# Kernel tuning notes

Measured on AMD Instinct MI355X. Metric: run time of the kernel, lower is better.

## Reference

```python
import jax, jax.numpy as jnp
import numpy as np

N_CONS = 100000
N_VARS = 200000
N_EDGES = 2000000
EMB = 64


def _emb(x, w0, b0, w1, b1):
    # Linear -> ReLU -> Linear -> ReLU
    h = jnp.maximum(x @ w0 + b0, 0.0)
    return jnp.maximum(h @ w1 + b1, 0.0)


def _bgc(left, src, dst, ef, right, lw, lb, ew, rw, fw, fb, ow0, ob0, ow1, ob1):
    # message: final(ReLU)(left_lin(right[dst]) + edge_lin(ef) + right_lin(left[src]))
    pre = right[dst] @ lw + lb + ef @ ew + left[src] @ rw          # [E, EMB]
    msg = jnp.maximum(pre, 0.0) @ fw + fb                          # [E, EMB]
    agg = jax.ops.segment_sum(msg, dst, num_segments=right.shape[0])  # [n_right, EMB]
    h = jnp.concatenate([agg, right], axis=-1)                     # [n_right, 2*EMB]
    return jnp.maximum(h @ ow0 + ob0, 0.0) @ ow1 + ob1


def setup_inputs() -> dict:
    key = jax.random.key(0)
    kit = iter(jax.random.split(key, 64))
    f32 = jnp.float32
    def W(i, o):
        return (jax.random.normal(next(kit), (i, o), f32) / np.float32(np.sqrt(i))).astype(f32)
    def B(o):
        return jnp.zeros((o,), f32)

    d = {}
    d['constraint_features'] = jax.random.normal(next(kit), (N_CONS, 5), f32)
    ei_c = jax.random.randint(next(kit), (N_EDGES,), 0, N_CONS)
    ei_v = jax.random.randint(next(kit), (N_EDGES,), 0, N_VARS)
    d['edge_indices'] = jnp.stack([ei_c, ei_v]).astype(jnp.int32)  # [2, E]
    d['edge_features'] = jax.random.normal(next(kit), (N_EDGES, 1), f32)
    d['variable_features'] = jax.random.normal(next(kit), (N_VARS, 19), f32)

    # cons / var embeddings
    d['cw0'], d['cb0'], d['cw1'], d['cb1'] = W(5, EMB), B(EMB), W(EMB, EMB), B(EMB)
    d['vw0'], d['vb0'], d['vw1'], d['vb1'] = W(19, EMB), B(EMB), W(EMB, EMB), B(EMB)
    # two bipartite convs
    for p in ('vc', 'cv'):
        d[p + '_lw'], d[p + '_lb'] = W(EMB, EMB), B(EMB)
        d[p + '_ew'] = W(1, EMB)
        d[p + '_rw'] = W(EMB, EMB)
        d[p + '_fw'], d[p + '_fb'] = W(EMB, EMB), B(EMB)
        d[p + '_ow0'], d[p + '_ob0'] = W(2 * EMB, EMB), B(EMB)
        d[p + '_ow1'], d[p + '_ob1'] = W(EMB, EMB), B(EMB)
    # policy head (final Linear has no bias)
    d['pw0'], d['pb0'], d['pw1'] = W(EMB, EMB), B(EMB), W(EMB, 1)
    # value head
    d['vhw0'], d['vhb0'], d['vhw1'], d['vhb1'] = W(EMB, EMB), B(EMB), W(EMB, 1), B(1)
    return d


def reference(constraint_features, edge_indices, edge_features, variable_features,
              cw0, cb0, cw1, cb1, vw0, vb0, vw1, vb1,
              vc_lw, vc_lb, vc_ew, vc_rw, vc_fw, vc_fb, vc_ow0, vc_ob0, vc_ow1, vc_ob1,
              cv_lw, cv_lb, cv_ew, cv_rw, cv_fw, cv_fb, cv_ow0, cv_ob0, cv_ow1, cv_ob1,
              pw0, pb0, pw1, vhw0, vhb0, vhw1, vhb1):
    cons_idx = edge_indices[0]
    var_idx = edge_indices[1]
    c = _emb(constraint_features, cw0, cb0, cw1, cb1)  # [n_cons, EMB]
    v = _emb(variable_features, vw0, vb0, vw1, vb1)    # [n_vars, EMB]
    # v -> c (reversed edges: src=var, dst=cons)
    c = _bgc(v, var_idx, cons_idx, edge_features, c,
             vc_lw, vc_lb, vc_ew, vc_rw, vc_fw, vc_fb, vc_ow0, vc_ob0, vc_ow1, vc_ob1)
    # c -> v (src=cons, dst=var)
    v = _bgc(c, cons_idx, var_idx, edge_features, v,
             cv_lw, cv_lb, cv_ew, cv_rw, cv_fw, cv_fb, cv_ow0, cv_ob0, cv_ow1, cv_ob1)
    policy = (jnp.maximum(v @ pw0 + pb0, 0.0) @ pw1).squeeze(-1)   # [n_vars]
    value = (jnp.maximum(v @ vhw0 + vhb0, 0.0) @ vhw1 + vhb1).squeeze(-1)  # [n_vars]
    return (value, policy)
```

## Files before the change

### kernel.cpp

```cpp
#include <hip/hip_runtime.h>

typedef unsigned short u16;

__device__ __forceinline__ float bf2f(u16 u) {
    return __uint_as_float(((unsigned int)u) << 16);
}
__device__ __forceinline__ u16 f2bf(float f) {
    unsigned int x = __float_as_uint(f);
    return (u16)((x + 0x7fffu + ((x >> 16) & 1u)) >> 16);
}

__device__ __forceinline__ void mm64(const float* A, const float* B, float* C, int lane)
{
    float bcol[64];
#pragma unroll
    for (int m = 0; m < 64; ++m) bcol[m] = B[m*64 + lane];
    for (int k = 0; k < 64; ++k) {
        float acc = 0.f;
#pragma unroll
        for (int m = 0; m < 64; ++m) acc = fmaf(A[k*64 + m], bcol[m], acc);
        C[k*64 + lane] = acc;
    }
}

__device__ __forceinline__ void vm64(const float* a, const float* B, const float* add,
                                     float* c, int lane)
{
    float acc = (add != 0) ? add[lane] : 0.f;
#pragma unroll
    for (int m = 0; m < 64; ++m) acc = fmaf(a[m], B[m*64 + lane], acc);
    c[lane] = acc;
}

__global__ __launch_bounds__(256) void prep_kernel(
    const float* vc_fw, const float* vc_fb, const float* vc_ow0,
    const float* vc_ow1, const float* vc_ob1,
    const float* cv_rw, const float* cv_fw, const float* cv_fb,
    const float* cv_ow0, const float* cv_ow1, const float* cv_ob1,
    const float* pw0, const float* pb0, const float* vhw0, const float* vhb0,
    float* Fc, float* gc, float* Hc, float* hc, float* Fv, float* gv,
    float* Pw, float* pbp, float* Vw, float* vbp)
{
    const int wv = threadIdx.x >> 6;
    const int lane = threadIdx.x & 63;
    if (wv == 0) {
        mm64(vc_fw, vc_ow0, Fc, lane);
        vm64(vc_fb, vc_ow0, 0, gc, lane);
    } else if (wv == 1) {
        mm64(vc_ow1, cv_rw, Hc, lane);
        vm64(vc_ob1, cv_rw, 0, hc, lane);
    } else if (wv == 2) {
        mm64(cv_fw, cv_ow0, Fv, lane);
        vm64(cv_fb, cv_ow0, 0, gv, lane);
    } else {
        mm64(cv_ow1, pw0, Pw, lane);
        vm64(cv_ob1, pw0, pb0, pbp, lane);
        mm64(cv_ow1, vhw0, Vw, lane);
        vm64(cv_ob1, vhw0, vhb0, vbp, lane);
    }
}

__global__ __launch_bounds__(256) void embc_kernel(
    const float* __restrict__ X,
    const float* __restrict__ W0, const float* __restrict__ B0,
    const float* __restrict__ W1, const float* __restrict__ B1,
    const float* __restrict__ LW, const float* __restrict__ LB,
    u16* __restrict__ c0out, float* __restrict__ RlOut, int M)
{
    const int lane = threadIdx.x & 63;
    const int wv   = threadIdx.x >> 6;
    __shared__ __align__(16) float xs[4][8*5];
    __shared__ __align__(16) float hb[4][8][64];
    __shared__ __align__(16) float yb[4][8][64];
    const int rowTile = (blockIdx.x*4 + wv)*8;

    for (int idx = lane; idx < 8*5; idx += 64) {
        long gi = (long)rowTile*5 + idx;
        xs[wv][idx] = (gi < (long)M*5) ? X[gi] : 0.f;
    }
    {
        float w0[5];
#pragma unroll
        for (int k = 0; k < 5; ++k) w0[k] = W0[k*64 + lane];
        const float b0 = B0[lane];
#pragma unroll
        for (int r = 0; r < 8; ++r) {
            float acc = b0;
#pragma unroll
            for (int k = 0; k < 5; ++k) acc = fmaf(xs[wv][r*5 + k], w0[k], acc);
            hb[wv][r][lane] = fmaxf(acc, 0.f);
        }
    }
    {
        float w1[64];
#pragma unroll
        for (int k = 0; k < 64; ++k) w1[k] = W1[k*64 + lane];
        const float b1 = B1[lane];
#pragma unroll
        for (int r = 0; r < 8; ++r) {
            float acc = b1;
#pragma unroll
            for (int k4 = 0; k4 < 16; ++k4) {
                float4 h4 = *(const float4*)&hb[wv][r][k4*4];
                acc = fmaf(h4.x, w1[k4*4+0], acc);
                acc = fmaf(h4.y, w1[k4*4+1], acc);
                acc = fmaf(h4.z, w1[k4*4+2], acc);
                acc = fmaf(h4.w, w1[k4*4+3], acc);
            }
            float y = fmaxf(acc, 0.f);
            yb[wv][r][lane] = y;
            int row = rowTile + r;
            if (row < M) c0out[(size_t)row*64 + lane] = f2bf(y);
        }
    }
    {
        float w[64];
#pragma unroll
        for (int k = 0; k < 64; ++k) w[k] = LW[k*64 + lane];
        const float bb = LB[lane];
#pragma unroll
        for (int r = 0; r < 8; ++r) {
            float acc = bb;
#pragma unroll
            for (int k4 = 0; k4 < 16; ++k4) {
                float4 y4 = *(const float4*)&yb[wv][r][k4*4];
                acc = fmaf(y4.x, w[k4*4+0], acc);
                acc = fmaf(y4.y, w[k4*4+1], acc);
                acc = fmaf(y4.z, w[k4*4+2], acc);
                acc = fmaf(y4.w, w[k4*4+3], acc);
            }
            int row = rowTile + r;
            if (row < M) RlOut[(size_t)row*64 + lane] = acc;
        }
    }
}

__global__ __launch_bounds__(256) void embv_kernel(
    const float* __restrict__ X,
    const float* __restrict__ W0, const float* __restrict__ B0,
    const float* __restrict__ W1, const float* __restrict__ B1,
    const float* __restrict__ RW,
    const float* __restrict__ LW, const float* __restrict__ LB,
    u16* __restrict__ v0out, u16* __restrict__ LsOut,
    float* __restrict__ RlOut, int M)
{
    const int lane = threadIdx.x & 63;
    const int wv   = threadIdx.x >> 6;
    __shared__ __align__(16) float xs[4][8*19];
    __shared__ __align__(16) float hb[4][8][64];
    __shared__ __align__(16) float yb[4][8][64];
    const int rowTile = (blockIdx.x*4 + wv)*8;

    for (int idx = lane; idx < 8*19; idx += 64) {
        long gi = (long)rowTile*19 + idx;
        xs[wv][idx] = (gi < (long)M*19) ? X[gi] : 0.f;
    }
    {
        float w0[19];
#pragma unroll
        for (int k = 0; k < 19; ++k) w0[k] = W0[k*64 + lane];
        const float b0 = B0[lane];
#pragma unroll
        for (int r = 0; r < 8; ++r) {
            float acc = b0;
#pragma unroll
            for (int k = 0; k < 19; ++k) acc = fmaf(xs[wv][r*19 + k], w0[k], acc);
            hb[wv][r][lane] = fmaxf(acc, 0.f);
        }
    }
    {
        float w1[64];
#pragma unroll
        for (int k = 0; k < 64; ++k) w1[k] = W1[k*64 + lane];
        const float b1 = B1[lane];
#pragma unroll
        for (int r = 0; r < 8; ++r) {
            float acc = b1;
#pragma unroll
            for (int k4 = 0; k4 < 16; ++k4) {
                float4 h4 = *(const float4*)&hb[wv][r][k4*4];
                acc = fmaf(h4.x, w1[k4*4+0], acc);
                acc = fmaf(h4.y, w1[k4*4+1], acc);
                acc = fmaf(h4.z, w1[k4*4+2], acc);
                acc = fmaf(h4.w, w1[k4*4+3], acc);
            }
            float y = fmaxf(acc, 0.f);
            yb[wv][r][lane] = y;
            int row = rowTile + r;
            if (row < M) v0out[(size_t)row*64 + lane] = f2bf(y);
        }
    }
    {
        float w[64];
#pragma unroll
        for (int k = 0; k < 64; ++k) w[k] = RW[k*64 + lane];
#pragma unroll
        for (int r = 0; r < 8; ++r) {
            float acc = 0.f;
#pragma unroll
            for (int k4 = 0; k4 < 16; ++k4) {
                float4 y4 = *(const float4*)&yb[wv][r][k4*4];
                acc = fmaf(y4.x, w[k4*4+0], acc);
                acc = fmaf(y4.y, w[k4*4+1], acc);
                acc = fmaf(y4.z, w[k4*4+2], acc);
                acc = fmaf(y4.w, w[k4*4+3], acc);
            }
            int row = rowTile + r;
            if (row < M) LsOut[(size_t)row*64 + lane] = f2bf(acc);
        }
    }
    {
        float w[64];
#pragma unroll
        for (int k = 0; k < 64; ++k) w[k] = LW[k*64 + lane];
        const float bb = LB[lane];
#pragma unroll
        for (int r = 0; r < 8; ++r) {
            float acc = bb;
#pragma unroll
            for (int k4 = 0; k4 < 16; ++k4) {
                float4 y4 = *(const float4*)&yb[wv][r][k4*4];
                acc = fmaf(y4.x, w[k4*4+0], acc);
                acc = fmaf(y4.y, w[k4*4+1], acc);
                acc = fmaf(y4.z, w[k4*4+2], acc);
                acc = fmaf(y4.w, w[k4*4+3], acc);
            }
            int row = rowTile + r;
            if (row < M) RlOut[(size_t)row*64 + lane] = acc;
        }
    }
}

__global__ __launch_bounds__(256) void hist2_kernel(
    const int* __restrict__ eic, const int* __restrict__ eiv,
    int* cntC, int* cntV, int E)
{
    int e = blockIdx.x*256 + threadIdx.x;
    if (e >= E) return;
    atomicAdd(&cntC[eic[e]], 1);
    atomicAdd(&cntV[eiv[e]], 1);
}

__global__ __launch_bounds__(256) void scan1_kernel(const int* __restrict__ in, int* blks, int N)
{
    __shared__ int sm[256];
    const int t = threadIdx.x;
    const int base = blockIdx.x*1024 + t*4;
    int s = 0;
#pragma unroll
    for (int i = 0; i < 4; ++i) { int idx = base + i; if (idx < N) s += in[idx]; }
    sm[t] = s; __syncthreads();
    for (int d = 128; d > 0; d >>= 1) { if (t < d) sm[t] += sm[t + d]; __syncthreads(); }
    if (t == 0) blks[blockIdx.x] = sm[0];
}

__global__ __launch_bounds__(256) void scan2_kernel(const int* __restrict__ blks, int* blkex, int nb)
{
    __shared__ int sm[1024];
    for (int i = threadIdx.x; i < nb; i += 256) sm[i] = blks[i];
    __syncthreads();
    if (threadIdx.x == 0) { int a = 0; for (int i = 0; i < nb; ++i) { int v = sm[i]; sm[i] = a; a += v; } }
    __syncthreads();
    for (int i = threadIdx.x; i < nb; i += 256) blkex[i] = sm[i];
}

__global__ __launch_bounds__(256) void scan3_kernel(
    const int* __restrict__ in, const int* __restrict__ blkex, int* out, int N)
{
    __shared__ int sm[256];
    const int t = threadIdx.x;
    const int base = blockIdx.x*1024 + t*4;
    int v[4]; int s = 0;
#pragma unroll
    for (int i = 0; i < 4; ++i) { int idx = base + i; v[i] = (idx < N) ? in[idx] : 0; s += v[i]; }
    sm[t] = s; __syncthreads();
    int x = s;
    for (int d = 1; d < 256; d <<= 1) {
        int y = (t >= d) ? sm[t - d] : 0;
        __syncthreads();
        x += y; sm[t] = x;
        __syncthreads();
    }
    int off0 = blkex[blockIdx.x] + (x - s);
#pragma unroll
    for (int i = 0; i < 4; ++i) {
        int idx = base + i;
        if (idx < N) {
            out[idx] = off0;
            off0 += v[i];
            if (idx == N - 1) out[N] = off0;
        }
    }
}

__global__ __launch_bounds__(256) void scatter2_kernel(
    const int* __restrict__ eic, const int* __restrict__ eiv,
    const float* __restrict__ ef,
    int* curC, int* curV, float2* __restrict__ bC, float2* __restrict__ bV, int E)
{
    int e = blockIdx.x*256 + threadIdx.x;
    if (e >= E) return;
    const int c = eic[e], v = eiv[e];
    const float f = ef[e];
    int pc = atomicAdd(&curC[c], 1);
    bC[pc] = make_float2(__int_as_float(v), f);
    int pv = atomicAdd(&curV[v], 1);
    bV[pv] = make_float2(__int_as_float(c), f);
}

__global__ __launch_bounds__(256) void agg_kernel(
    const int* __restrict__ off, const float2* __restrict__ bucket,
    float* RlA, const u16* __restrict__ Lsb,
    const float* __restrict__ ew, int N)
{
    const int node = blockIdx.x*4 + (threadIdx.x >> 6);
    if (node >= N) return;
    const int lane = threadIdx.x & 63;
    const int s0 = off[node];
    const int e1 = off[node + 1];
    const float rl = RlA[(size_t)node*64 + lane];
    const float w  = ew[lane];

    float acc = 0.f;
    int j = s0;
    for (; j + 8 <= e1; j += 8) {
        float2 q0 = bucket[j+0], q1 = bucket[j+1], q2 = bucket[j+2], q3 = bucket[j+3];
        float2 q4 = bucket[j+4], q5 = bucket[j+5], q6 = bucket[j+6], q7 = bucket[j+7];
        float l0 = bf2f(Lsb[(size_t)__float_as_int(q0.x)*64 + lane]);
        float l1 = bf2f(Lsb[(size_t)__float_as_int(q1.x)*64 + lane]);
        float l2 = bf2f(Lsb[(size_t)__float_as_int(q2.x)*64 + lane]);
        float l3 = bf2f(Lsb[(size_t)__float_as_int(q3.x)*64 + lane]);
        float l4 = bf2f(Lsb[(size_t)__float_as_int(q4.x)*64 + lane]);
        float l5 = bf2f(Lsb[(size_t)__float_as_int(q5.x)*64 + lane]);
        float l6 = bf2f(Lsb[(size_t)__float_as_int(q6.x)*64 + lane]);
        float l7 = bf2f(Lsb[(size_t)__float_as_int(q7.x)*64 + lane]);
        acc += fmaxf(fmaf(q0.y, w, rl + l0), 0.f);
        acc += fmaxf(fmaf(q1.y, w, rl + l1), 0.f);
        acc += fmaxf(fmaf(q2.y, w, rl + l2), 0.f);
        acc += fmaxf(fmaf(q3.y, w, rl + l3), 0.f);
        acc += fmaxf(fmaf(q4.y, w, rl + l4), 0.f);
        acc += fmaxf(fmaf(q5.y, w, rl + l5), 0.f);
        acc += fmaxf(fmaf(q6.y, w, rl + l6), 0.f);
        acc += fmaxf(fmaf(q7.y, w, rl + l7), 0.f);
    }
    for (; j < e1; ++j) {
        float2 q = bucket[j];
        float l = bf2f(Lsb[(size_t)__float_as_int(q.x)*64 + lane]);
        acc += fmaxf(fmaf(q.y, w, rl + l), 0.f);
    }
    RlA[(size_t)node*64 + lane] = acc;
}

__global__ __launch_bounds__(256, 1) void consupd_kernel(
    const float* __restrict__ aggpre, const u16* __restrict__ c0,
    const int* __restrict__ off,
    const float* __restrict__ Fc, const float* __restrict__ OW0B,
    const float* __restrict__ gc, const float* __restrict__ ob0,
    const float* __restrict__ Hc, const float* __restrict__ hc,
    u16* __restrict__ LsOut, int M)
{
    const int lane = threadIdx.x & 63;
    const int wv   = threadIdx.x >> 6;
    __shared__ __align__(16) float xs[4][8][64];
    __shared__ __align__(16) float cs[4][8][64];
    const int rowTile = (blockIdx.x*4 + wv)*8;

    float degv[8];
#pragma unroll
    for (int r = 0; r < 8; ++r) {
        int row = rowTile + r;
        int grow = (row < M) ? row : (M - 1);
        xs[wv][r][lane] = aggpre[(size_t)grow*64 + lane];
        cs[wv][r][lane] = bf2f(c0[(size_t)grow*64 + lane]);
        degv[r] = (float)(off[grow + 1] - off[grow]);
    }
    {
        float wa[64], wb[64];
#pragma unroll
        for (int k = 0; k < 64; ++k) { wa[k] = Fc[k*64 + lane]; wb[k] = OW0B[k*64 + lane]; }
        const float g_l = gc[lane], b_l = ob0[lane];
#pragma unroll
        for (int r = 0; r < 8; ++r) {
            float acc = fmaf(degv[r], g_l, b_l);
#pragma unroll
            for (int k4 = 0; k4 < 16; ++k4) {
                float4 x4 = *(const float4*)&xs[wv][r][k4*4];
                float4 c4 = *(const float4*)&cs[wv][r][k4*4];
                acc = fmaf(x4.x, wa[k4*4+0], acc); acc = fmaf(c4.x, wb[k4*4+0], acc);
                acc = fmaf(x4.y, wa[k4*4+1], acc); acc = fmaf(c4.y, wb[k4*4+1], acc);
                acc = fmaf(x4.z, wa[k4*4+2], acc); acc = fmaf(c4.z, wb[k4*4+2], acc);
                acc = fmaf(x4.w, wa[k4*4+3], acc); acc = fmaf(c4.w, wb[k4*4+3], acc);
            }
            xs[wv][r][lane] = fmaxf(acc, 0.f);
        }
    }
    {
        float wh[64];
#pragma unroll
        for (int k = 0; k < 64; ++k) wh[k] = Hc[k*64 + lane];
        const float h_l = hc[lane];
#pragma unroll
        for (int r = 0; r < 8; ++r) {
            float acc = h_l;
#pragma unroll
            for (int k4 = 0; k4 < 16; ++k4) {
                float4 u4 = *(const float4*)&xs[wv][r][k4*4];
                acc = fmaf(u4.x, wh[k4*4+0], acc);
                acc = fmaf(u4.y, wh[k4*4+1], acc);
                acc = fmaf(u4.z, wh[k4*4+2], acc);
                acc = fmaf(u4.w, wh[k4*4+3], acc);
            }
            int row = rowTile + r;
            if (row < M) LsOut[(size_t)row*64 + lane] = f2bf(acc);
        }
    }
}

__global__ __launch_bounds__(256, 1) void varupdhead_kernel(
    const float* __restrict__ aggpre, const u16* __restrict__ v0,
    const int* __restrict__ off,
    const float* __restrict__ Fv, const float* __restrict__ OW0B,
    const float* __restrict__ gv, const float* __restrict__ ob0,
    const float* __restrict__ Pw, const float* __restrict__ pbp, const float* __restrict__ pw1,
    const float* __restrict__ Vw, const float* __restrict__ vbp, const float* __restrict__ vw1,
    const float* __restrict__ vb1,
    float* __restrict__ out, int M)
{
    const int lane = threadIdx.x & 63;
    const int wv   = threadIdx.x >> 6;
    __shared__ __align__(16) float xs[4][8][64];
    __shared__ __align__(16) float cs[4][8][64];
    const int rowTile = (blockIdx.x*4 + wv)*8;

    float degv[8];
#pragma unroll
    for (int r = 0; r < 8; ++r) {
        int row = rowTile + r;
        int grow = (row < M) ? row : (M - 1);
        xs[wv][r][lane] = aggpre[(size_t)grow*64 + lane];
        cs[wv][r][lane] = bf2f(v0[(size_t)grow*64 + lane]);
        degv[r] = (float)(off[grow + 1] - off[grow]);
    }
    {
        float wa[64], wb[64];
#pragma unroll
        for (int k = 0; k < 64; ++k) { wa[k] = Fv[k*64 + lane]; wb[k] = OW0B[k*64 + lane]; }
        const float g_l = gv[lane], b_l = ob0[lane];
#pragma unroll
        for (int r = 0; r < 8; ++r) {
            float acc = fmaf(degv[r], g_l, b_l);
#pragma unroll
            for (int k4 = 0; k4 < 16; ++k4) {
                float4 x4 = *(const float4*)&xs[wv][r][k4*4];
                float4 c4 = *(const float4*)&cs[wv][r][k4*4];
                acc = fmaf(x4.x, wa[k4*4+0], acc); acc = fmaf(c4.x, wb[k4*4+0], acc);
                acc = fmaf(x4.y, wa[k4*4+1], acc); acc = fmaf(c4.y, wb[k4*4+1], acc);
                acc = fmaf(x4.z, wa[k4*4+2], acc); acc = fmaf(c4.z, wb[k4*4+2], acc);
                acc = fmaf(x4.w, wa[k4*4+3], acc); acc = fmaf(c4.w, wb[k4*4+3], acc);
            }
            xs[wv][r][lane] = fmaxf(acc, 0.f);
        }
    }
    {
        float wp[64], wq[64];
#pragma unroll
        for (int k = 0; k < 64; ++k) { wp[k] = Pw[k*64 + lane]; wq[k] = Vw[k*64 + lane]; }
        const float pb_l = pbp[lane], vb_l = vbp[lane];
        const float p1w = pw1[lane], v1w = vw1[lane];
        const float vbias = vb1[0];
#pragma unroll
        for (int r = 0; r < 8; ++r) {
            float tp = pb_l, tv = vb_l;
#pragma unroll
            for (int k4 = 0; k4 < 16; ++k4) {
                float4 u4 = *(const float4*)&xs[wv][r][k4*4];
                tp = fmaf(u4.x, wp[k4*4+0], tp); tv = fmaf(u4.x, wq[k4*4+0], tv);
                tp = fmaf(u4.y, wp[k4*4+1], tp); tv = fmaf(u4.y, wq[k4*4+1], tv);
                tp = fmaf(u4.z, wp[k4*4+2], tp); tv = fmaf(u4.z, wq[k4*4+2], tv);
                tp = fmaf(u4.w, wp[k4*4+3], tp); tv = fmaf(u4.w, wq[k4*4+3], tv);
            }
            tp = fmaxf(tp, 0.f) * p1w;
            tv = fmaxf(tv, 0.f) * v1w;
#pragma unroll
            for (int m = 32; m >= 1; m >>= 1) {
                tp += __shfl_xor(tp, m, 64);
                tv += __shfl_xor(tv, m, 64);
            }
            int row = rowTile + r;
            if (lane == 0 && row < M) {
                out[row]     = tv + vbias;
                out[M + row] = tp;
            }
        }
    }
}

#define AL256(x) (((x) + 255) & ~(size_t)255)

extern "C" void kernel_launch(void* const* d_in, const int* in_sizes, int n_in,
                              void* d_out, int out_size, void* d_ws, size_t ws_size,
                              hipStream_t stream)
{
    const float* cf  = (const float*)d_in[0];
    const int*   ei  = (const int*)  d_in[1];
    const float* ef  = (const float*)d_in[2];
    const float* vf  = (const float*)d_in[3];

    const float* cw0 = (const float*)d_in[4];
    const float* cb0 = (const float*)d_in[5];
    const float* cw1 = (const float*)d_in[6];
    const float* cb1 = (const float*)d_in[7];
    const float* vw0 = (const float*)d_in[8];
    const float* vb0 = (const float*)d_in[9];
    const float* vw1 = (const float*)d_in[10];
    const float* vb1 = (const float*)d_in[11];

    const float* vc_lw  = (const float*)d_in[12];
    const float* vc_lb  = (const float*)d_in[13];
    const float* vc_ew  = (const float*)d_in[14];
    const float* vc_rw  = (const float*)d_in[15];
    const float* vc_fw  = (const float*)d_in[16];
    const float* vc_fb  = (const float*)d_in[17];
    const float* vc_ow0 = (const float*)d_in[18];
    const float* vc_ob0 = (const float*)d_in[19];
    const float* vc_ow1 = (const float*)d_in[20];
    const float* vc_ob1 = (const float*)d_in[21];

    const float* cv_lw  = (const float*)d_in[22];
    const float* cv_lb  = (const float*)d_in[23];
    const float* cv_ew  = (const float*)d_in[24];
    const float* cv_rw  = (const float*)d_in[25];
    const float* cv_fw  = (const float*)d_in[26];
    const float* cv_fb  = (const float*)d_in[27];
    const float* cv_ow0 = (const float*)d_in[28];
    const float* cv_ob0 = (const float*)d_in[29];
    const float* cv_ow1 = (const float*)d_in[30];
    const float* cv_ob1 = (const float*)d_in[31];

    const float* pw0  = (const float*)d_in[32];
    const float* pb0  = (const float*)d_in[33];
    const float* pw1  = (const float*)d_in[34];
    const float* vhw0 = (const float*)d_in[35];
    const float* vhb0 = (const float*)d_in[36];
    const float* vhw1 = (const float*)d_in[37];
    const float* vhb1 = (const float*)d_in[38];

    const int NC = in_sizes[0] / 5;
    const int E  = in_sizes[1] / 2;
    const int NV = in_sizes[3] / 19;
    const int* eic = ei;
    const int* eiv = ei + E;

    char* base = (char*)d_ws;
    size_t o = 0;
    float*  RlC = (float*)(base + o);  o += AL256((size_t)NC*64*4);
    u16*    c0b = (u16*)  (base + o);  o += AL256((size_t)NC*64*2);
    u16*    LsC = (u16*)  (base + o);  o += AL256((size_t)NC*64*2);
    float*  RlV = (float*)(base + o);  o += AL256((size_t)NV*64*4);
    u16*    v0b = (u16*)  (base + o);  o += AL256((size_t)NV*64*2);
    u16*    LsV = (u16*)  (base + o);  o += AL256((size_t)NV*64*2);
    float2* bktC = (float2*)(base + o); o += AL256((size_t)E*8);
    float2* bktV = (float2*)(base + o); o += AL256((size_t)E*8);
    int* cntC = (int*)(base + o);  o += AL256((size_t)NC*4);
    int* offC = (int*)(base + o);  o += AL256(((size_t)NC + 1)*4);
    int* cntV = (int*)(base + o);  o += AL256((size_t)NV*4);
    int* offV = (int*)(base + o);  o += AL256(((size_t)NV + 1)*4);
    int* blks = (int*)(base + o);  o += AL256((size_t)1024*4);
    int* blkex= (int*)(base + o);  o += AL256((size_t)1024*4);
    float* Fc  = (float*)(base + o); o += AL256((size_t)4096*4);
    float* Hc  = (float*)(base + o); o += AL256((size_t)4096*4);
    float* Fv  = (float*)(base + o); o += AL256((size_t)4096*4);
    float* Pw  = (float*)(base + o); o += AL256((size_t)4096*4);
    float* Vw  = (float*)(base + o); o += AL256((size_t)4096*4);
    float* gc  = (float*)(base + o); o += AL256((size_t)64*4);
    float* hc  = (float*)(base + o); o += AL256((size_t)64*4);
    float* gv  = (float*)(base + o); o += AL256((size_t)64*4);
    float* pbp = (float*)(base + o); o += AL256((size_t)64*4);
    float* vbp = (float*)(base + o); o += AL256((size_t)64*4);

    if (o > ws_size) return;

    dim3 blk(256);
    dim3 gRowsC((unsigned)((NC + 31) / 32));
    dim3 gRowsV((unsigned)((NV + 31) / 32));
    dim3 gNodeC((unsigned)((NC + 3) / 4));
    dim3 gNodeV((unsigned)((NV + 3) / 4));
    dim3 gE((unsigned)((E + 255) / 256));
    const int nbC = (NC + 1023) / 1024;
    const int nbV = (NV + 1023) / 1024;

    (void)hipMemsetAsync(cntC, 0, (size_t)NC*4, stream);
    (void)hipMemsetAsync(cntV, 0, (size_t)NV*4, stream);
    hist2_kernel<<<gE, blk, 0, stream>>>(eic, eiv, cntC, cntV, E);
    scan1_kernel<<<dim3(nbC), blk, 0, stream>>>(cntC, blks, NC);
    scan2_kernel<<<dim3(1),   blk, 0, stream>>>(blks, blkex, nbC);
    scan3_kernel<<<dim3(nbC), blk, 0, stream>>>(cntC, blkex, offC, NC);
    scan1_kernel<<<dim3(nbV), blk, 0, stream>>>(cntV, blks, NV);
    scan2_kernel<<<dim3(1),   blk, 0, stream>>>(blks, blkex, nbV);
    scan3_kernel<<<dim3(nbV), blk, 0, stream>>>(cntV, blkex, offV, NV);

    prep_kernel<<<dim3(1), blk, 0, stream>>>(
        vc_fw, vc_fb, vc_ow0, vc_ow1, vc_ob1,
        cv_rw, cv_fw, cv_fb, cv_ow0, cv_ow1, cv_ob1,
        pw0, pb0, vhw0, vhb0,
        Fc, gc, Hc, hc, Fv, gv, Pw, pbp, Vw, vbp);

    embc_kernel<<<gRowsC, blk, 0, stream>>>(cf, cw0, cb0, cw1, cb1,
                                            vc_lw, vc_lb, c0b, RlC, NC);
    embv_kernel<<<gRowsV, blk, 0, stream>>>(vf, vw0, vb0, vw1, vb1,
                                            vc_rw, cv_lw, cv_lb, v0b, LsV, RlV, NV);

    (void)hipMemcpyAsync(cntC, offC, (size_t)NC*4, hipMemcpyDeviceToDevice, stream);
    (void)hipMemcpyAsync(cntV, offV, (size_t)NV*4, hipMemcpyDeviceToDevice, stream);
    scatter2_kernel<<<gE, blk, 0, stream>>>(eic, eiv, ef, cntC, cntV, bktC, bktV, E);

    agg_kernel<<<gNodeC, blk, 0, stream>>>(offC, bktC, RlC, LsV, vc_ew, NC);
    consupd_kernel<<<gRowsC, blk, 0, stream>>>(RlC, c0b, offC,
                                               Fc, vc_ow0 + 64*64, gc, vc_ob0,
                                               Hc, hc, LsC, NC);

    agg_kernel<<<gNodeV, blk, 0, stream>>>(offV, bktV, RlV, LsC, cv_ew, NV);
    varupdhead_kernel<<<gRowsV, blk, 0, stream>>>(RlV, v0b, offV,
                                                  Fv, cv_ow0 + 64*64, gv, cv_ob0,
                                                  Pw, pbp, pw1, Vw, vbp, vhw1, vhb1,
                                                  (float*)d_out, NV);
}
```

Before: 1.216 ms.

## Replace per-node CSR with coarse 128-node buckets and LDS-atomic aggregation

Edges are now bucketed by groups of 128 destination nodes instead of being fully sorted per node. The multi-kernel prefix scan becomes one single-block coarse scan, and the scatter atomics go to far fewer counters. Aggregation runs one block per bucket and accumulates into shared memory with LDS atomics. The local node index is packed into the low 7 bits of the edge feature and rl is stored as bf16, which slightly lowers precision. LDS atomic contention and a single-block serial scan over roughly 1600 buckets are the added costs.

```diff
diff --git a/kernel.cpp b/kernel.cpp
--- a/kernel.cpp
+++ b/kernel.cpp
@@ -1,6 +1,9 @@
 #include <hip/hip_runtime.h>
 
 typedef unsigned short u16;
+
+#define RN  128
+#define RSH 7
 
 __device__ __forceinline__ float bf2f(u16 u) {
     return __uint_as_float(((unsigned int)u) << 16);
@@ -241,119 +244,117 @@
     atomicAdd(&cntV[eiv[e]], 1);
 }
 
-__global__ __launch_bounds__(256) void scan1_kernel(const int* __restrict__ in, int* blks, int N)
-{
-    __shared__ int sm[256];
-    const int t = threadIdx.x;
-    const int base = blockIdx.x*1024 + t*4;
-    int s = 0;
-#pragma unroll
-    for (int i = 0; i < 4; ++i) { int idx = base + i; if (idx < N) s += in[idx]; }
-    sm[t] = s; __syncthreads();
-    for (int d = 128; d > 0; d >>= 1) { if (t < d) sm[t] += sm[t + d]; __syncthreads(); }
-    if (t == 0) blks[blockIdx.x] = sm[0];
-}
-
-__global__ __launch_bounds__(256) void scan2_kernel(const int* __restrict__ blks, int* blkex, int nb)
-{
-    __shared__ int sm[1024];
-    for (int i = threadIdx.x; i < nb; i += 256) sm[i] = blks[i];
+__global__ __launch_bounds__(256) void coarse_kernel(
+    const int* __restrict__ cnt, int N, int nb, int* cOff, int* cur)
+{
+    __shared__ int cs[2049];
+    for (int i = threadIdx.x; i < nb; i += 256) {
+        int s = 0;
+        int basei = i << RSH;
+        int lim = N - basei; if (lim > RN) lim = RN;
+        for (int j = 0; j < lim; ++j) s += cnt[basei + j];
+        cs[i] = s;
+    }
     __syncthreads();
-    if (threadIdx.x == 0) { int a = 0; for (int i = 0; i < nb; ++i) { int v = sm[i]; sm[i] = a; a += v; } }
+    if (threadIdx.x == 0) {
+        int a = 0;
+        for (int i = 0; i < nb; ++i) { int t = cs[i]; cs[i] = a; a += t; }
+        cs[nb] = a;
+    }
     __syncthreads();
-    for (int i = threadIdx.x; i < nb; i += 256) blkex[i] = sm[i];
-}
-
-__global__ __launch_bounds__(256) void scan3_kernel(
-    const int* __restrict__ in, const int* __restrict__ blkex, int* out, int N)
-{
-    __shared__ int sm[256];
-    const int t = threadIdx.x;
-    const int base = blockIdx.x*1024 + t*4;
-    int v[4]; int s = 0;
-#pragma unroll
-    for (int i = 0; i < 4; ++i) { int idx = base + i; v[i] = (idx < N) ? in[idx] : 0; s += v[i]; }
-    sm[t] = s; __syncthreads();
-    int x = s;
-    for (int d = 1; d < 256; d <<= 1) {
-        int y = (t >= d) ? sm[t - d] : 0;
-        __syncthreads();
-        x += y; sm[t] = x;
-        __syncthreads();
-    }
-    int off0 = blkex[blockIdx.x] + (x - s);
-#pragma unroll
-    for (int i = 0; i < 4; ++i) {
-        int idx = base + i;
-        if (idx < N) {
-            out[idx] = off0;
-            off0 += v[i];
-            if (idx == N - 1) out[N] = off0;
-        }
-    }
-}
-
-__global__ __launch_bounds__(256) void scatter2_kernel(
+    for (int i = threadIdx.x; i < nb; i += 256) { cOff[i] = cs[i]; cur[i] = cs[i]; }
+    if (threadIdx.x == 0) cOff[nb] = cs[nb];
+}
+
+__global__ __launch_bounds__(256) void cscatter_kernel(
     const int* __restrict__ eic, const int* __restrict__ eiv,
     const float* __restrict__ ef,
-    int* curC, int* curV, float2* __restrict__ bC, float2* __restrict__ bV, int E)
+    int* curC, int* curV, uint2* __restrict__ bC, uint2* __restrict__ bV, int E)
 {
     int e = blockIdx.x*256 + threadIdx.x;
     if (e >= E) return;
     const int c = eic[e], v = eiv[e];
-    const float f = ef[e];
-    int pc = atomicAdd(&curC[c], 1);
-    bC[pc] = make_float2(__int_as_float(v), f);
-    int pv = atomicAdd(&curV[v], 1);
-    bV[pv] = make_float2(__int_as_float(c), f);
-}
-
-__global__ __launch_bounds__(256) void agg_kernel(
-    const int* __restrict__ off, const float2* __restrict__ bucket,
+    const unsigned fb = __float_as_uint(ef[e]) & 0xFFFFFF80u;
+    int pc = atomicAdd(&curC[c >> RSH], 1);
+    bC[pc] = make_uint2((unsigned)v, fb | (unsigned)(c & (RN - 1)));
+    int pv = atomicAdd(&curV[v >> RSH], 1);
+    bV[pv] = make_uint2((unsigned)c, fb | (unsigned)(v & (RN - 1)));
+}
+
+__global__ __launch_bounds__(256) void aggb_kernel(
+    const int* __restrict__ cOff, const uint2* __restrict__ bucket,
     float* RlA, const u16* __restrict__ Lsb,
     const float* __restrict__ ew, int N)
 {
-    const int node = blockIdx.x*4 + (threadIdx.x >> 6);
-    if (node >= N) return;
+    const int b = blockIdx.x;
     const int lane = threadIdx.x & 63;
-    const int s0 = off[node];
-    const int e1 = off[node + 1];
-    const float rl = RlA[(size_t)node*64 + lane];
-    const float w  = ew[lane];
-
-    float acc = 0.f;
-    int j = s0;
-    for (; j + 8 <= e1; j += 8) {
-        float2 q0 = bucket[j+0], q1 = bucket[j+1], q2 = bucket[j+2], q3 = bucket[j+3];
-        float2 q4 = bucket[j+4], q5 = bucket[j+5], q6 = bucket[j+6], q7 = bucket[j+7];
-        float l0 = bf2f(Lsb[(size_t)__float_as_int(q0.x)*64 + lane]);
-        float l1 = bf2f(Lsb[(size_t)__float_as_int(q1.x)*64 + lane]);
-        float l2 = bf2f(Lsb[(size_t)__float_as_int(q2.x)*64 + lane]);
-        float l3 = bf2f(Lsb[(size_t)__float_as_int(q3.x)*64 + lane]);
-        float l4 = bf2f(Lsb[(size_t)__float_as_int(q4.x)*64 + lane]);
-        float l5 = bf2f(Lsb[(size_t)__float_as_int(q5.x)*64 + lane]);
-        float l6 = bf2f(Lsb[(size_t)__float_as_int(q6.x)*64 + lane]);
-        float l7 = bf2f(Lsb[(size_t)__float_as_int(q7.x)*64 + lane]);
-        acc += fmaxf(fmaf(q0.y, w, rl + l0), 0.f);
-        acc += fmaxf(fmaf(q1.y, w, rl + l1), 0.f);
-        acc += fmaxf(fmaf(q2.y, w, rl + l2), 0.f);
-        acc += fmaxf(fmaf(q3.y, w, rl + l3), 0.f);
-        acc += fmaxf(fmaf(q4.y, w, rl + l4), 0.f);
-        acc += fmaxf(fmaf(q5.y, w, rl + l5), 0.f);
-        acc += fmaxf(fmaf(q6.y, w, rl + l6), 0.f);
-        acc += fmaxf(fmaf(q7.y, w, rl + l7), 0.f);
-    }
-    for (; j < e1; ++j) {
-        float2 q = bucket[j];
-        float l = bf2f(Lsb[(size_t)__float_as_int(q.x)*64 + lane]);
-        acc += fmaxf(fmaf(q.y, w, rl + l), 0.f);
-    }
-    RlA[(size_t)node*64 + lane] = acc;
+    const int wv   = threadIdx.x >> 6;
+    const int n0 = b << RSH;
+    int nn = N - n0; if (nn > RN) nn = RN;
+
+    __shared__ float accS[RN][64];
+    __shared__ u16   rlS[RN][64];
+
+    for (int r = wv; r < nn; r += 4) {
+        float rl = RlA[(size_t)(n0 + r)*64 + lane];
+        rlS[r][lane]  = f2bf(rl);
+        accS[r][lane] = 0.f;
+    }
+    __syncthreads();
+
+    const float w = ew[lane];
+    const int e0 = cOff[b], e1 = cOff[b + 1];
+
+    for (int base = e0 + wv*8; base < e1; base += 32) {
+        int m = e1 - base; if (m > 8) m = 8;
+        if (m == 8) {
+            uint2 q0 = bucket[base+0], q1 = bucket[base+1], q2 = bucket[base+2], q3 = bucket[base+3];
+            uint2 q4 = bucket[base+4], q5 = bucket[base+5], q6 = bucket[base+6], q7 = bucket[base+7];
+            float l0 = bf2f(Lsb[(size_t)q0.x*64 + lane]);
+            float l1 = bf2f(Lsb[(size_t)q1.x*64 + lane]);
+            float l2 = bf2f(Lsb[(size_t)q2.x*64 + lane]);
+            float l3 = bf2f(Lsb[(size_t)q3.x*64 + lane]);
+            float l4 = bf2f(Lsb[(size_t)q4.x*64 + lane]);
+            float l5 = bf2f(Lsb[(size_t)q5.x*64 + lane]);
+            float l6 = bf2f(Lsb[(size_t)q6.x*64 + lane]);
+            float l7 = bf2f(Lsb[(size_t)q7.x*64 + lane]);
+            int d0 = q0.y & 127, d1 = q1.y & 127, d2 = q2.y & 127, d3 = q3.y & 127;
+            int d4 = q4.y & 127, d5 = q5.y & 127, d6 = q6.y & 127, d7 = q7.y & 127;
+            float f0 = __uint_as_float(q0.y & 0xFFFFFF80u);
+            float f1 = __uint_as_float(q1.y & 0xFFFFFF80u);
+            float f2 = __uint_as_float(q2.y & 0xFFFFFF80u);
+            float f3 = __uint_as_float(q3.y & 0xFFFFFF80u);
+            float f4 = __uint_as_float(q4.y & 0xFFFFFF80u);
+            float f5 = __uint_as_float(q5.y & 0xFFFFFF80u);
+            float f6 = __uint_as_float(q6.y & 0xFFFFFF80u);
+            float f7 = __uint_as_float(q7.y & 0xFFFFFF80u);
+            atomicAdd(&accS[d0][lane], fmaxf(fmaf(f0, w, bf2f(rlS[d0][lane]) + l0), 0.f));
+            atomicAdd(&accS[d1][lane], fmaxf(fmaf(f1, w, bf2f(rlS[d1][lane]) + l1), 0.f));
+            atomicAdd(&accS[d2][lane], fmaxf(fmaf(f2, w, bf2f(rlS[d2][lane]) + l2), 0.f));
+            atomicAdd(&accS[d3][lane], fmaxf(fmaf(f3, w, bf2f(rlS[d3][lane]) + l3), 0.f));
+            atomicAdd(&accS[d4][lane], fmaxf(fmaf(f4, w, bf2f(rlS[d4][lane]) + l4), 0.f));
+            atomicAdd(&accS[d5][lane], fmaxf(fmaf(f5, w, bf2f(rlS[d5][lane]) + l5), 0.f));
+            atomicAdd(&accS[d6][lane], fmaxf(fmaf(f6, w, bf2f(rlS[d6][lane]) + l6), 0.f));
+            atomicAdd(&accS[d7][lane], fmaxf(fmaf(f7, w, bf2f(rlS[d7][lane]) + l7), 0.f));
+        } else {
+            for (int i = 0; i < m; ++i) {
+                uint2 q = bucket[base + i];
+                float l = bf2f(Lsb[(size_t)q.x*64 + lane]);
+                int   d = q.y & 127;
+                float f = __uint_as_float(q.y & 0xFFFFFF80u);
+                atomicAdd(&accS[d][lane], fmaxf(fmaf(f, w, bf2f(rlS[d][lane]) + l), 0.f));
+            }
+        }
+    }
+    __syncthreads();
+
+    for (int r = wv; r < nn; r += 4)
+        RlA[(size_t)(n0 + r)*64 + lane] = accS[r][lane];
 }
 
 __global__ __launch_bounds__(256, 1) void consupd_kernel(
     const float* __restrict__ aggpre, const u16* __restrict__ c0,
-    const int* __restrict__ off,
+    const int* __restrict__ deg,
     const float* __restrict__ Fc, const float* __restrict__ OW0B,
     const float* __restrict__ gc, const float* __restrict__ ob0,
     const float* __restrict__ Hc, const float* __restrict__ hc,
@@ -372,7 +373,7 @@
         int grow = (row < M) ? row : (M - 1);
         xs[wv][r][lane] = aggpre[(size_t)grow*64 + lane];
         cs[wv][r][lane] = bf2f(c0[(size_t)grow*64 + lane]);
-        degv[r] = (float)(off[grow + 1] - off[grow]);
+        degv[r] = (float)deg[grow];
     }
     {
         float wa[64], wb[64];
@@ -418,7 +419,7 @@
 
 __global__ __launch_bounds__(256, 1) void varupdhead_kernel(
     const float* __restrict__ aggpre, const u16* __restrict__ v0,
-    const int* __restrict__ off,
+    const int* __restrict__ deg,
     const float* __restrict__ Fv, const float* __restrict__ OW0B,
     const float* __restrict__ gv, const float* __restrict__ ob0,
     const float* __restrict__ Pw, const float* __restrict__ pbp, const float* __restrict__ pw1,
@@ -439,7 +440,7 @@
         int grow = (row < M) ? row : (M - 1);
         xs[wv][r][lane] = aggpre[(size_t)grow*64 + lane];
         cs[wv][r][lane] = bf2f(v0[(size_t)grow*64 + lane]);
-        degv[r] = (float)(off[grow + 1] - off[grow]);
+        degv[r] = (float)deg[grow];
     }
     {
         float wa[64], wb[64];
@@ -551,6 +552,9 @@
     const int* eic = ei;
     const int* eiv = ei + E;
 
+    const int nbC = (NC + RN - 1) >> RSH;
+    const int nbV = (NV + RN - 1) >> RSH;
+
     char* base = (char*)d_ws;
     size_t o = 0;
     float*  RlC = (float*)(base + o);  o += AL256((size_t)NC*64*4);
@@ -559,14 +563,14 @@
     float*  RlV = (float*)(base + o);  o += AL256((size_t)NV*64*4);
     u16*    v0b = (u16*)  (base + o);  o += AL256((size_t)NV*64*2);
     u16*    LsV = (u16*)  (base + o);  o += AL256((size_t)NV*64*2);
-    float2* bktC = (float2*)(base + o); o += AL256((size_t)E*8);
-    float2* bktV = (float2*)(base + o); o += AL256((size_t)E*8);
-    int* cntC = (int*)(base + o);  o += AL256((size_t)NC*4);
-    int* offC = (int*)(base + o);  o += AL256(((size_t)NC + 1)*4);
-    int* cntV = (int*)(base + o);  o += AL256((size_t)NV*4);
-    int* offV = (int*)(base + o);  o += AL256(((size_t)NV + 1)*4);
-    int* blks = (int*)(base + o);  o += AL256((size_t)1024*4);
-    int* blkex= (int*)(base + o);  o += AL256((size_t)1024*4);
+    uint2*  bktC = (uint2*)(base + o); o += AL256((size_t)E*8);
+    uint2*  bktV = (uint2*)(base + o); o += AL256((size_t)E*8);
+    int* cntC  = (int*)(base + o);  o += AL256((size_t)NC*4);
+    int* cntV  = (int*)(base + o);  o += AL256((size_t)NV*4);
+    int* cOffC = (int*)(base + o);  o += AL256(((size_t)nbC + 1)*4);
+    int* curC  = (int*)(base + o);  o += AL256((size_t)nbC*4);
+    int* cOffV = (int*)(base + o);  o += AL256(((size_t)nbV + 1)*4);
+    int* curV  = (int*)(base + o);  o += AL256((size_t)nbV*4);
     float* Fc  = (float*)(base + o); o += AL256((size_t)4096*4);
     float* Hc  = (float*)(base + o); o += AL256((size_t)4096*4);
     float* Fv  = (float*)(base + o); o += AL256((size_t)4096*4);
@@ -583,21 +587,13 @@
     dim3 blk(256);
     dim3 gRowsC((unsigned)((NC + 31) / 32));
     dim3 gRowsV((unsigned)((NV + 31) / 32));
-    dim3 gNodeC((unsigned)((NC + 3) / 4));
-    dim3 gNodeV((unsigned)((NV + 3) / 4));
     dim3 gE((unsigned)((E + 255) / 256));
-    const int nbC = (NC + 1023) / 1024;
-    const int nbV = (NV + 1023) / 1024;
 
     (void)hipMemsetAsync(cntC, 0, (size_t)NC*4, stream);
     (void)hipMemsetAsync(cntV, 0, (size_t)NV*4, stream);
     hist2_kernel<<<gE, blk, 0, stream>>>(eic, eiv, cntC, cntV, E);
-    scan1_kernel<<<dim3(nbC), blk, 0, stream>>>(cntC, blks, NC);
-    scan2_kernel<<<dim3(1),   blk, 0, stream>>>(blks, blkex, nbC);
-    scan3_kernel<<<dim3(nbC), blk, 0, stream>>>(cntC, blkex, offC, NC);
-    scan1_kernel<<<dim3(nbV), blk, 0, stream>>>(cntV, blks, NV);
-    scan2_kernel<<<dim3(1),   blk, 0, stream>>>(blks, blkex, nbV);
-    scan3_kernel<<<dim3(nbV), blk, 0, stream>>>(cntV, blkex, offV, NV);
+    coarse_kernel<<<dim3(1), blk, 0, stream>>>(cntC, NC, nbC, cOffC, curC);
+    coarse_kernel<<<dim3(1), blk, 0, stream>>>(cntV, NV, nbV, cOffV, curV);
 
     prep_kernel<<<dim3(1), blk, 0, stream>>>(
         vc_fw, vc_fb, vc_ow0, vc_ow1, vc_ob1,
@@ -610,17 +606,15 @@
     embv_kernel<<<gRowsV, blk, 0, stream>>>(vf, vw0, vb0, vw1, vb1,
                                             vc_rw, cv_lw, cv_lb, v0b, LsV, RlV, NV);
 
-    (void)hipMemcpyAsync(cntC, offC, (size_t)NC*4, hipMemcpyDeviceToDevice, stream);
-    (void)hipMemcpyAsync(cntV, offV, (size_t)NV*4, hipMemcpyDeviceToDevice, stream);
-    scatter2_kernel<<<gE, blk, 0, stream>>>(eic, eiv, ef, cntC, cntV, bktC, bktV, E);
-
-    agg_kernel<<<gNodeC, blk, 0, stream>>>(offC, bktC, RlC, LsV, vc_ew, NC);
-    consupd_kernel<<<gRowsC, blk, 0, stream>>>(RlC, c0b, offC,
+    cscatter_kernel<<<gE, blk, 0, stream>>>(eic, eiv, ef, curC, curV, bktC, bktV, E);
+
+    aggb_kernel<<<dim3((unsigned)nbC), blk, 0, stream>>>(cOffC, bktC, RlC, LsV, vc_ew, NC);
+    consupd_kernel<<<gRowsC, blk, 0, stream>>>(RlC, c0b, cntC,
                                                Fc, vc_ow0 + 64*64, gc, vc_ob0,
                                                Hc, hc, LsC, NC);
 
-    agg_kernel<<<gNodeV, blk, 0, stream>>>(offV, bktV, RlV, LsC, cv_ew, NV);
-    varupdhead_kernel<<<gRowsV, blk, 0, stream>>>(RlV, v0b, offV,
+    aggb_kernel<<<dim3((unsigned)nbV), blk, 0, stream>>>(cOffV, bktV, RlV, LsC, cv_ew, NV);
+    varupdhead_kernel<<<gRowsV, blk, 0, stream>>>(RlV, v0b, cntV,
                                                   Fv, cv_ow0 + 64*64, gv, cv_ob0,
                                                   Pw, pbp, pw1, Vw, vbp, vhw1, vhb1,
                                                   (float*)d_out, NV);
```

Result: slower. 2.862 ms (+135.4%).
